# Kernel optimization log

Measured on AMD Instinct MI355X. Metric: run time of the kernel, lower is better.

## Reference

```python
import jax, jax.numpy as jnp
import numpy as np

N_NODES = 100000


def gcn_conv(x, W, b, row, col, n):
    """PyG GCNConv: linear transform, then symmetric-normalized aggregation
    with self-loops (add_self_loops=True, normalize=True, bias=True)."""
    h = x @ W  # [N, F_out]
    e_ones = jnp.ones(row.shape[0], dtype=x.dtype)
    # in-degree of target nodes, +1 for the implicit self-loop
    deg = jax.ops.segment_sum(e_ones, col, num_segments=n) + 1.0
    dinv = jax.lax.rsqrt(deg)  # deg >= 1 always
    norm = dinv[row] * dinv[col]  # [E]
    msg = h[row] * norm[:, None]  # gather + scale, [E, F_out]
    agg = jax.ops.segment_sum(msg, col, num_segments=n)  # scatter-add to targets
    agg = agg + h * (dinv * dinv)[:, None]  # self-loop contribution
    return agg + b


def setup_inputs() -> dict:
    key = jax.random.key(0)
    k1, k2, k3, k4 = jax.random.split(key, 4)
    F_in, F_hid, F_out = 512, 64, 40
    E = 1_600_000
    x = jax.random.normal(k1, (N_NODES, F_in), dtype=jnp.float32)
    edge_index = jax.random.randint(k2, (2, E), 0, N_NODES, dtype=jnp.int64)
    # Glorot-ish scaling for weights
    W1 = jax.random.normal(k3, (F_in, F_hid), dtype=jnp.float32) * (1.0 / np.sqrt(F_in))
    W2 = jax.random.normal(k4, (F_hid, F_out), dtype=jnp.float32) * (1.0 / np.sqrt(F_hid))
    b1 = jnp.zeros((F_hid,), dtype=jnp.float32)
    b2 = jnp.zeros((F_out,), dtype=jnp.float32)
    return {"x": x, "edge_index": edge_index, "W1": W1, "b1": b1, "W2": W2, "b2": b2}


def reference(x, edge_index, W1, b1, W2, b2):
    n = x.shape[0]
    row, col = edge_index[0], edge_index[1]
    h = jax.nn.relu(gcn_conv(x, W1, b1, row, col, n))
    # dropout is identity in eval mode (training=False)
    h = gcn_conv(h, W2, b2, row, col, n)
    return jax.nn.log_softmax(h, axis=1)
```

## Files before the change

kernel.cpp:

```cpp
#include <hip/hip_runtime.h>
#include <math.h>


#define FIN 512
#define FHID 64
#define FOUT 40

#define BSH 8
#define BN 256
#define BCAP 5120
#define EPW 4096

typedef __attribute__((ext_vector_type(8))) short short8;
typedef __attribute__((ext_vector_type(4))) float f32x4;
typedef unsigned short ushort_t;
typedef unsigned int uint_t;

__device__ __forceinline__ ushort_t bf16_rn(float f) {
    union { float f; uint_t u; } v; v.f = f;
    uint_t r = v.u + 0x7FFF + ((v.u >> 16) & 1);
    return (ushort_t)(r >> 16);
}
__device__ __forceinline__ uint_t pack_bf16(float a, float b) {
    return (uint_t)bf16_rn(a) | ((uint_t)bf16_rn(b) << 16);
}
__device__ __forceinline__ float bf16_to_f(ushort_t u) {
    union { uint_t i; float f; } t; t.i = ((uint_t)u) << 16; return t.f;
}
__device__ __forceinline__ void add8(float* acc, uint4 g) {
    acc[0] += __uint_as_float(g.x << 16);
    acc[1] += __uint_as_float(g.x & 0xFFFF0000u);
    acc[2] += __uint_as_float(g.y << 16);
    acc[3] += __uint_as_float(g.y & 0xFFFF0000u);
    acc[4] += __uint_as_float(g.z << 16);
    acc[5] += __uint_as_float(g.z & 0xFFFF0000u);
    acc[6] += __uint_as_float(g.w << 16);
    acc[7] += __uint_as_float(g.w & 0xFFFF0000u);
}

__global__ __launch_bounds__(256) void bucket_scatter_kernel(
    const int* __restrict__ row, const int* __restrict__ col,
    int* __restrict__ gcur, uint_t* __restrict__ stage, int E) {
    __shared__ uint_t cnt[512];
    __shared__ uint_t base[512];
    int tid = threadIdx.x;
    cnt[tid] = 0; cnt[tid + 256] = 0;
    __syncthreads();
    int e0 = blockIdx.x * EPW;
    int creg[16];
#pragma unroll
    for (int it = 0; it < 16; ++it) {
        int e = e0 + it * 256 + tid;
        creg[it] = (e < E) ? col[e] : -1;
        if (e < E) atomicAdd(&cnt[((uint_t)creg[it]) >> BSH], 1u);
    }
    __syncthreads();
    uint_t c0 = cnt[tid], c1 = cnt[tid + 256];
    base[tid] = c0 ? (uint_t)atomicAdd(&gcur[tid], (int)c0) : 0u;
    base[tid + 256] = c1 ? (uint_t)atomicAdd(&gcur[tid + 256], (int)c1) : 0u;
    __syncthreads();
    cnt[tid] = 0; cnt[tid + 256] = 0;
    __syncthreads();
#pragma unroll
    for (int it = 0; it < 16; ++it) {
        int e = e0 + it * 256 + tid;
        if (e < E) {
            int c = creg[it];
            int r = row[e];
            int b = c >> BSH;
            uint_t slot = base[b] + atomicAdd(&cnt[b], 1u);
            stage[(size_t)b * BCAP + slot] = ((uint_t)r << BSH) | (uint_t)(c & (BN - 1));
        }
    }
}

__global__ void scan2_kernel(int* __restrict__ bsums, int nb) {
    __shared__ int tmp[512];
    int tid = threadIdx.x;
    int v = (tid < nb) ? bsums[tid] : 0;
    tmp[tid] = v;
    __syncthreads();
    for (int off = 1; off < 512; off <<= 1) {
        int t = (tid >= off) ? tmp[tid - off] : 0;
        __syncthreads();
        tmp[tid] += t;
        __syncthreads();
    }
    if (tid < nb) bsums[tid] = tmp[tid] - v;
}

__global__ __launch_bounds__(256) void bucket_place_kernel(
    const int* __restrict__ gcur, const uint_t* __restrict__ stage,
    int* __restrict__ sSrc, int* __restrict__ deg, float* __restrict__ dinv,
    int* __restrict__ offs, int n) {
    __shared__ int lcnt[256];
    __shared__ int ltmp[256];
    __shared__ int lpos[256];
    int b = blockIdx.x, tid = threadIdx.x;
    int nodeBase = b << BSH;
    int bucketBase = gcur[b];
    int cnt = gcur[b + 1] - bucketBase;
    lcnt[tid] = 0;
    __syncthreads();
    const uint_t* sp = &stage[(size_t)b * BCAP];
    for (int i = tid; i < cnt; i += 256)
        atomicAdd(&lcnt[sp[i] & (BN - 1)], 1);
    __syncthreads();
    int v = lcnt[tid];
    ltmp[tid] = v;
    __syncthreads();
    for (int off = 1; off < 256; off <<= 1) {
        int t = (tid >= off) ? ltmp[tid - off] : 0;
        __syncthreads();
        ltmp[tid] += t;
        __syncthreads();
    }
    int gofs = bucketBase + ltmp[tid] - v;
    int node = nodeBase + tid;
    if (node < n) {
        deg[node] = v;
        dinv[node] = rsqrtf((float)v + 1.0f);
        offs[node] = gofs;
    }
    lpos[tid] = gofs;
    __syncthreads();
    for (int i = tid; i < cnt; i += 256) {
        uint_t w = sp[i];
        int pos = atomicAdd(&lpos[w & (BN - 1)], 1);
        sSrc[pos] = (int)(w >> BSH);
    }
}

__global__ void wprep_kernel(const float* __restrict__ W1, const float* __restrict__ W2,
                             ushort_t* __restrict__ Wt,
                             ushort_t* __restrict__ w2hi, ushort_t* __restrict__ w2lo) {
    int idx = blockIdx.x * 256 + threadIdx.x;
    if (idx < 32768) {
        int nrow = idx >> 9;
        int k = idx & 511;
        Wt[idx] = bf16_rn(W1[k * 64 + nrow]);
    } else if (idx < 32768 + 3072) {
        int i = idx - 32768;
        int j = i >> 6, k = i & 63;
        float w = (j < FOUT) ? W2[k * FOUT + j] : 0.f;
        ushort_t h = bf16_rn(w);
        w2hi[i] = h;
        w2lo[i] = bf16_rn(w - bf16_to_f(h));
    }
}

#define LDA 72
#define LDB 72
__global__ __launch_bounds__(256) void gemm1_kernel(
    const float* __restrict__ x, const ushort_t* __restrict__ Wt,
    const float* __restrict__ dinv, ushort_t* __restrict__ h1b, int n) {
    __shared__ ushort_t lA[128 * LDA];
    __shared__ ushort_t lB[64 * LDB];

    int tid = threadIdx.x;
    int wave = tid >> 6, lane = tid & 63;
    int quad = lane >> 4, m16 = lane & 15;
    int node0 = blockIdx.x * 128;

    int r0 = tid >> 4, k4 = tid & 15;
    int nr0 = tid >> 3, seg = tid & 7;

    f32x4 zero = {0.f, 0.f, 0.f, 0.f};
    f32x4 acc[2][4];
#pragma unroll
    for (int mt = 0; mt < 2; ++mt)
#pragma unroll
        for (int nt = 0; nt < 4; ++nt) acc[mt][nt] = zero;

    float4 ra[8];
    uint4 rb[2];

#pragma unroll
    for (int i = 0; i < 8; ++i) {
        int node = node0 + r0 + i * 16;
        float4 v = make_float4(0.f, 0.f, 0.f, 0.f);
        if (node < n) v = *reinterpret_cast<const float4*>(&x[(size_t)node * FIN + k4 * 4]);
        ra[i] = v;
    }
#pragma unroll
    for (int i = 0; i < 2; ++i)
        rb[i] = *reinterpret_cast<const uint4*>(&Wt[(size_t)(nr0 + i * 32) * FIN + seg * 8]);

    for (int c = 0; c < 8; ++c) {
#pragma unroll
        for (int i = 0; i < 8; ++i)
            *reinterpret_cast<uint2*>(&lA[(r0 + i * 16) * LDA + k4 * 4]) =
                make_uint2(pack_bf16(ra[i].x, ra[i].y), pack_bf16(ra[i].z, ra[i].w));
#pragma unroll
        for (int i = 0; i < 2; ++i)
            *reinterpret_cast<uint4*>(&lB[(nr0 + i * 32) * LDB + seg * 8]) = rb[i];
        __syncthreads();

        if (c < 7) {
            int kc = (c + 1) * 64;
#pragma unroll
            for (int i = 0; i < 8; ++i) {
                int node = node0 + r0 + i * 16;
                float4 v = make_float4(0.f, 0.f, 0.f, 0.f);
                if (node < n)
                    v = *reinterpret_cast<const float4*>(&x[(size_t)node * FIN + kc + k4 * 4]);
                ra[i] = v;
            }
#pragma unroll
            for (int i = 0; i < 2; ++i)
                rb[i] = *reinterpret_cast<const uint4*>(
                    &Wt[(size_t)(nr0 + i * 32) * FIN + kc + seg * 8]);
        }

#pragma unroll
        for (int kk = 0; kk < 2; ++kk) {
            short8 a[2], b[4];
#pragma unroll
            for (int mt = 0; mt < 2; ++mt)
                a[mt] = *reinterpret_cast<const short8*>(
                    &lA[(wave * 32 + mt * 16 + m16) * LDA + kk * 32 + quad * 8]);
#pragma unroll
            for (int nt = 0; nt < 4; ++nt)
                b[nt] = *reinterpret_cast<const short8*>(
                    &lB[(nt * 16 + m16) * LDB + kk * 32 + quad * 8]);
#pragma unroll
            for (int mt = 0; mt < 2; ++mt)
#pragma unroll
                for (int nt = 0; nt < 4; ++nt)
                    acc[mt][nt] = __builtin_amdgcn_mfma_f32_16x16x32_bf16(
                        a[mt], b[nt], acc[mt][nt], 0, 0, 0);
        }
        __syncthreads();
    }

#pragma unroll
    for (int mt = 0; mt < 2; ++mt) {
#pragma unroll
        for (int reg = 0; reg < 4; ++reg) {
            int node = node0 + wave * 32 + mt * 16 + quad * 4 + reg;
            if (node < n) {
                float di = dinv[node];
#pragma unroll
                for (int nt = 0; nt < 4; ++nt)
                    h1b[(size_t)node * 64 + nt * 16 + m16] =
                        bf16_rn(acc[mt][nt][reg] * di);
            }
        }
    }
}

template <int MODE>
__global__ __launch_bounds__(256) void agg_kernel(
    const int* __restrict__ offs, const int* __restrict__ deg,
    const int* __restrict__ sSrc, const ushort_t* __restrict__ src,
    const float* __restrict__ dinv, const float* __restrict__ b1,
    ushort_t* __restrict__ dst, int n) {
    __shared__ float lacc[8][4 * 68];
    __shared__ float lb1[64];
    int tid = threadIdx.x;
    if (MODE == 0 && tid < 64) lb1[tid] = b1[tid];

    int wv = tid >> 6, lane = tid & 63;
    int half = lane >> 5;
    int l32 = lane & 31;
    int e4 = l32 >> 3, c = l32 & 7;
    int slot = wv * 2 + half;
    int node = blockIdx.x * 8 + slot;
    bool valid = node < n;
    int start = valid ? offs[node] : 0;
    int cnt = valid ? deg[node] : 0;

    float acc[8];
#pragma unroll
    for (int j = 0; j < 8; ++j) acc[j] = 0.f;

    for (int base = 0; base < cnt; base += 16) {
        int i0 = base + e4, i1 = i0 + 4, i2 = i0 + 8, i3 = i0 + 12;
        int s0 = (i0 < cnt) ? sSrc[start + i0] : n;
        int s1 = (i1 < cnt) ? sSrc[start + i1] : n;
        int s2 = (i2 < cnt) ? sSrc[start + i2] : n;
        int s3 = (i3 < cnt) ? sSrc[start + i3] : n;
        uint4 g0 = *reinterpret_cast<const uint4*>(&src[(size_t)s0 * 64 + c * 8]);
        uint4 g1 = *reinterpret_cast<const uint4*>(&src[(size_t)s1 * 64 + c * 8]);
        uint4 g2 = *reinterpret_cast<const uint4*>(&src[(size_t)s2 * 64 + c * 8]);
        uint4 g3 = *reinterpret_cast<const uint4*>(&src[(size_t)s3 * 64 + c * 8]);
        add8(acc, g0);
        add8(acc, g1);
        add8(acc, g2);
        add8(acc, g3);
    }

    {
        float* lw = &lacc[slot][e4 * 68 + c * 8];
        *reinterpret_cast<float4*>(lw) = make_float4(acc[0], acc[1], acc[2], acc[3]);
        *reinterpret_cast<float4*>(lw + 4) = make_float4(acc[4], acc[5], acc[6], acc[7]);
    }
    __syncthreads();

    int s = tid >> 5;
    int fp = tid & 31;
    int enode = blockIdx.x * 8 + s;
    if (enode < n) {
        float sum0 = 0.f, sum1 = 0.f;
#pragma unroll
        for (int g = 0; g < 4; ++g) {
            sum0 += lacc[s][g * 68 + fp * 2];
            sum1 += lacc[s][g * 68 + fp * 2 + 1];
        }
        float di = dinv[enode];
        uint_t sv = *reinterpret_cast<const uint_t*>(&src[(size_t)enode * 64 + fp * 2]);
        float self0 = __uint_as_float(sv << 16);
        float self1 = __uint_as_float(sv & 0xFFFF0000u);
        float v0 = (sum0 + self0) * di;
        float v1 = (sum1 + self1) * di;
        if (MODE == 0) {
            v0 = fmaxf(v0 + lb1[fp * 2], 0.f) * di;
            v1 = fmaxf(v1 + lb1[fp * 2 + 1], 0.f) * di;
        }
        *reinterpret_cast<uint_t*>(&dst[(size_t)enode * 64 + fp * 2]) = pack_bf16(v0, v1);
    }
}

#define LDC 72
__global__ __launch_bounds__(256) void gemm2sm_kernel(
    const ushort_t* __restrict__ A, const ushort_t* __restrict__ w2hi,
    const ushort_t* __restrict__ w2lo, const float* __restrict__ b2,
    float* __restrict__ out, int n) {
    __shared__ ushort_t lA[128 * LDC];
    __shared__ ushort_t lBh[48 * LDC];
    __shared__ ushort_t lBl[48 * LDC];

    int tid = threadIdx.x;
    int wave = tid >> 6, lane = tid & 63;
    int quad = lane >> 4, m16 = lane & 15;
    int node0 = blockIdx.x * 128;

    {
        int r = tid & 127, part = tid >> 7;
        int node = node0 + r;
        uint4 z = make_uint4(0u, 0u, 0u, 0u);
        const uint4* sp = reinterpret_cast<const uint4*>(&A[(size_t)node * 64 + part * 32]);
#pragma unroll
        for (int i = 0; i < 4; ++i) {
            uint4 v = (node < n) ? sp[i] : z;
            *reinterpret_cast<uint4*>(&lA[r * LDC + part * 32 + i * 8]) = v;
        }
    }
    for (int i = tid; i < 384; i += 256) {
        int row = i >> 3, seg = i & 7;
        *reinterpret_cast<uint4*>(&lBh[row * LDC + seg * 8]) =
            reinterpret_cast<const uint4*>(w2hi)[i];
        *reinterpret_cast<uint4*>(&lBl[row * LDC + seg * 8]) =
            reinterpret_cast<const uint4*>(w2lo)[i];
    }
    float rb2_0 = b2[m16];
    float rb2_1 = b2[16 + m16];
    float rb2_2 = (m16 < 8) ? b2[32 + m16] : 0.f;
    __syncthreads();

    f32x4 zero = {0.f, 0.f, 0.f, 0.f};
    f32x4 acc[2][3];
#pragma unroll
    for (int mt = 0; mt < 2; ++mt)
#pragma unroll
        for (int nt = 0; nt < 3; ++nt) acc[mt][nt] = zero;

#pragma unroll
    for (int kk = 0; kk < 2; ++kk) {
        short8 a[2], bh[3], bl[3];
#pragma unroll
        for (int mt = 0; mt < 2; ++mt)
            a[mt] = *reinterpret_cast<const short8*>(
                &lA[(wave * 32 + mt * 16 + m16) * LDC + kk * 32 + quad * 8]);
#pragma unroll
        for (int nt = 0; nt < 3; ++nt) {
            bh[nt] = *reinterpret_cast<const short8*>(
                &lBh[(nt * 16 + m16) * LDC + kk * 32 + quad * 8]);
            bl[nt] = *reinterpret_cast<const short8*>(
                &lBl[(nt * 16 + m16) * LDC + kk * 32 + quad * 8]);
        }
#pragma unroll
        for (int mt = 0; mt < 2; ++mt)
#pragma unroll
            for (int nt = 0; nt < 3; ++nt) {
                acc[mt][nt] = __builtin_amdgcn_mfma_f32_16x16x32_bf16(
                    a[mt], bh[nt], acc[mt][nt], 0, 0, 0);
                acc[mt][nt] = __builtin_amdgcn_mfma_f32_16x16x32_bf16(
                    a[mt], bl[nt], acc[mt][nt], 0, 0, 0);
            }
    }

    bool c2 = (m16 < 8);
#pragma unroll
    for (int mt = 0; mt < 2; ++mt) {
#pragma unroll
        for (int reg = 0; reg < 4; ++reg) {
            int node = node0 + wave * 32 + mt * 16 + quad * 4 + reg;
            float r0 = acc[mt][0][reg] + rb2_0;
            float r1 = acc[mt][1][reg] + rb2_1;
            float r2 = acc[mt][2][reg] + rb2_2;
            float pm = fmaxf(fmaxf(r0, r1), c2 ? r2 : -INFINITY);
#pragma unroll
            for (int mask = 1; mask <= 8; mask <<= 1)
                pm = fmaxf(pm, __shfl_xor(pm, mask));
            float s = expf(r0 - pm) + expf(r1 - pm) + (c2 ? expf(r2 - pm) : 0.f);
#pragma unroll
            for (int mask = 1; mask <= 8; mask <<= 1)
                s += __shfl_xor(s, mask);
            float ls = logf(s) + pm;
            if (node < n) {
                float* op = &out[(size_t)node * FOUT];
                op[m16] = r0 - ls;
                op[16 + m16] = r1 - ls;
                if (c2) op[32 + m16] = r2 - ls;
            }
        }
    }
}

extern "C" void kernel_launch(void* const* d_in, const int* in_sizes, int n_in,
                              void* d_out, int out_size, void* d_ws, size_t ws_size,
                              hipStream_t stream) {
    const float* x  = (const float*)d_in[0];
    const int*   ei = (const int*)d_in[1];
    const float* W1 = (const float*)d_in[2];
    const float* b1 = (const float*)d_in[3];
    const float* W2 = (const float*)d_in[4];
    const float* b2 = (const float*)d_in[5];
    float* out = (float*)d_out;

    int n = in_sizes[0] / FIN;
    int E = in_sizes[1] / 2;
    const int* row = ei;
    const int* col = ei + E;

    int* wsi = (int*)d_ws;
    const size_t NR = 100352;
    int*      deg   = wsi;
    float*    dinv  = (float*)(wsi + NR);
    int*      offs  = wsi + 2 * NR;
    int*      gcur  = wsi + 3 * NR;
    ushort_t* Wt    = (ushort_t*)(wsi + 3 * NR + 512);
    ushort_t* w2hi  = Wt + 64 * 512;
    ushort_t* w2lo  = w2hi + 48 * 64;
    uint_t*   stage = (uint_t*)(w2lo + 48 * 64);
    int*      sSrc  = (int*)(stage + (size_t)512 * BCAP);
    ushort_t* h1b   = (ushort_t*)(sSrc + (size_t)E);
    ushort_t* h1a   = h1b + (size_t)(n + 1) * 64;
    ushort_t* Abuf  = h1b;

    int NBUCK = (n + BN - 1) >> BSH;
    int nwg1 = (E + EPW - 1) / EPW;

    hipMemsetAsync(gcur, 0, 512 * 4, stream);
    hipMemsetAsync(h1b + (size_t)n * 64, 0, 128, stream);
    hipMemsetAsync(h1a + (size_t)n * 64, 0, 128, stream);
    bucket_scatter_kernel<<<nwg1, 256, 0, stream>>>(row, col, gcur, stage, E);
    scan2_kernel<<<1, 512, 0, stream>>>(gcur, 512);
    bucket_place_kernel<<<NBUCK, 256, 0, stream>>>(gcur, stage, sSrc, deg, dinv, offs, n);

    wprep_kernel<<<140, 256, 0, stream>>>(W1, W2, Wt, w2hi, w2lo);

    gemm1_kernel<<<(n + 127) / 128, 256, 0, stream>>>(x, Wt, dinv, h1b, n);

    agg_kernel<0><<<(n + 7) / 8, 256, 0, stream>>>(offs, deg, sSrc, h1b, dinv, b1, h1a, n);

    agg_kernel<1><<<(n + 7) / 8, 256, 0, stream>>>(offs, deg, sSrc, h1a, dinv, b1, Abuf, n);

    gemm2sm_kernel<<<(n + 127) / 128, 256, 0, stream>>>(Abuf, w2hi, w2lo, b2, out, n);
}
```

Measured before the change: 445.9 us.

## Fold memsets and bucket scan into existing kernels; add nontemporal loads/stores

Replaces the three hipMemsetAsync calls by zeroing the bucket counters and sentinel rows inside the weight-prep kernel, which now runs first. The separate single-block scan kernel is removed, and every bucket_place block recomputes the 512-entry prefix sum itself. Streaming accesses (x, edge indices, stage, sSrc, gemm2 input and output) now use nontemporal load/store builtins to reduce cache pollution. This cuts launch count and small dispatch gaps, at the cost of redundant scan work in each place block.

```diff
diff --git a/kernel.cpp b/kernel.cpp
--- a/kernel.cpp
+++ b/kernel.cpp
@@ -13,8 +13,10 @@
 
 typedef __attribute__((ext_vector_type(8))) short short8;
 typedef __attribute__((ext_vector_type(4))) float f32x4;
+typedef __attribute__((ext_vector_type(4))) float float4v;
 typedef unsigned short ushort_t;
 typedef unsigned int uint_t;
+typedef __attribute__((ext_vector_type(4))) uint_t uint4v;
 
 __device__ __forceinline__ ushort_t bf16_rn(float f) {
     union { float f; uint_t u; } v; v.f = f;
@@ -38,103 +40,14 @@
     acc[7] += __uint_as_float(g.w & 0xFFFF0000u);
 }
 
-__global__ __launch_bounds__(256) void bucket_scatter_kernel(
-    const int* __restrict__ row, const int* __restrict__ col,
-    int* __restrict__ gcur, uint_t* __restrict__ stage, int E) {
-    __shared__ uint_t cnt[512];
-    __shared__ uint_t base[512];
-    int tid = threadIdx.x;
-    cnt[tid] = 0; cnt[tid + 256] = 0;
-    __syncthreads();
-    int e0 = blockIdx.x * EPW;
-    int creg[16];
-#pragma unroll
-    for (int it = 0; it < 16; ++it) {
-        int e = e0 + it * 256 + tid;
-        creg[it] = (e < E) ? col[e] : -1;
-        if (e < E) atomicAdd(&cnt[((uint_t)creg[it]) >> BSH], 1u);
-    }
-    __syncthreads();
-    uint_t c0 = cnt[tid], c1 = cnt[tid + 256];
-    base[tid] = c0 ? (uint_t)atomicAdd(&gcur[tid], (int)c0) : 0u;
-    base[tid + 256] = c1 ? (uint_t)atomicAdd(&gcur[tid + 256], (int)c1) : 0u;
-    __syncthreads();
-    cnt[tid] = 0; cnt[tid + 256] = 0;
-    __syncthreads();
-#pragma unroll
-    for (int it = 0; it < 16; ++it) {
-        int e = e0 + it * 256 + tid;
-        if (e < E) {
-            int c = creg[it];
-            int r = row[e];
-            int b = c >> BSH;
-            uint_t slot = base[b] + atomicAdd(&cnt[b], 1u);
-            stage[(size_t)b * BCAP + slot] = ((uint_t)r << BSH) | (uint_t)(c & (BN - 1));
-        }
-    }
-}
-
-__global__ void scan2_kernel(int* __restrict__ bsums, int nb) {
-    __shared__ int tmp[512];
-    int tid = threadIdx.x;
-    int v = (tid < nb) ? bsums[tid] : 0;
-    tmp[tid] = v;
-    __syncthreads();
-    for (int off = 1; off < 512; off <<= 1) {
-        int t = (tid >= off) ? tmp[tid - off] : 0;
-        __syncthreads();
-        tmp[tid] += t;
-        __syncthreads();
-    }
-    if (tid < nb) bsums[tid] = tmp[tid] - v;
-}
-
-__global__ __launch_bounds__(256) void bucket_place_kernel(
-    const int* __restrict__ gcur, const uint_t* __restrict__ stage,
-    int* __restrict__ sSrc, int* __restrict__ deg, float* __restrict__ dinv,
-    int* __restrict__ offs, int n) {
-    __shared__ int lcnt[256];
-    __shared__ int ltmp[256];
-    __shared__ int lpos[256];
-    int b = blockIdx.x, tid = threadIdx.x;
-    int nodeBase = b << BSH;
-    int bucketBase = gcur[b];
-    int cnt = gcur[b + 1] - bucketBase;
-    lcnt[tid] = 0;
-    __syncthreads();
-    const uint_t* sp = &stage[(size_t)b * BCAP];
-    for (int i = tid; i < cnt; i += 256)
-        atomicAdd(&lcnt[sp[i] & (BN - 1)], 1);
-    __syncthreads();
-    int v = lcnt[tid];
-    ltmp[tid] = v;
-    __syncthreads();
-    for (int off = 1; off < 256; off <<= 1) {
-        int t = (tid >= off) ? ltmp[tid - off] : 0;
-        __syncthreads();
-        ltmp[tid] += t;
-        __syncthreads();
-    }
-    int gofs = bucketBase + ltmp[tid] - v;
-    int node = nodeBase + tid;
-    if (node < n) {
-        deg[node] = v;
-        dinv[node] = rsqrtf((float)v + 1.0f);
-        offs[node] = gofs;
-    }
-    lpos[tid] = gofs;
-    __syncthreads();
-    for (int i = tid; i < cnt; i += 256) {
-        uint_t w = sp[i];
-        int pos = atomicAdd(&lpos[w & (BN - 1)], 1);
-        sSrc[pos] = (int)(w >> BSH);
-    }
-}
-
 __global__ void wprep_kernel(const float* __restrict__ W1, const float* __restrict__ W2,
                              ushort_t* __restrict__ Wt,
-                             ushort_t* __restrict__ w2hi, ushort_t* __restrict__ w2lo) {
+                             ushort_t* __restrict__ w2hi, ushort_t* __restrict__ w2lo,
+                             int* __restrict__ gcur,
+                             ushort_t* __restrict__ sent1, ushort_t* __restrict__ sent2) {
     int idx = blockIdx.x * 256 + threadIdx.x;
+    if (idx < 512) gcur[idx] = 0;
+    if (idx < 64) { sent1[idx] = 0; sent2[idx] = 0; }
     if (idx < 32768) {
         int nrow = idx >> 9;
         int k = idx & 511;
@@ -149,6 +62,96 @@
     }
 }
 
+__global__ __launch_bounds__(256) void bucket_scatter_kernel(
+    const int* __restrict__ row, const int* __restrict__ col,
+    int* __restrict__ gcur, uint_t* __restrict__ stage, int E) {
+    __shared__ uint_t cnt[512];
+    __shared__ uint_t base[512];
+    int tid = threadIdx.x;
+    cnt[tid] = 0; cnt[tid + 256] = 0;
+    __syncthreads();
+    int e0 = blockIdx.x * EPW;
+    int creg[16];
+#pragma unroll
+    for (int it = 0; it < 16; ++it) {
+        int e = e0 + it * 256 + tid;
+        creg[it] = (e < E) ? __builtin_nontemporal_load(&col[e]) : -1;
+        if (e < E) atomicAdd(&cnt[((uint_t)creg[it]) >> BSH], 1u);
+    }
+    __syncthreads();
+    uint_t c0 = cnt[tid], c1 = cnt[tid + 256];
+    base[tid] = c0 ? (uint_t)atomicAdd(&gcur[tid], (int)c0) : 0u;
+    base[tid + 256] = c1 ? (uint_t)atomicAdd(&gcur[tid + 256], (int)c1) : 0u;
+    __syncthreads();
+    cnt[tid] = 0; cnt[tid + 256] = 0;
+    __syncthreads();
+#pragma unroll
+    for (int it = 0; it < 16; ++it) {
+        int e = e0 + it * 256 + tid;
+        if (e < E) {
+            int c = creg[it];
+            int r = __builtin_nontemporal_load(&row[e]);
+            int b = c >> BSH;
+            uint_t slot = base[b] + atomicAdd(&cnt[b], 1u);
+            stage[(size_t)b * BCAP + slot] = ((uint_t)r << BSH) | (uint_t)(c & (BN - 1));
+        }
+    }
+}
+
+__global__ __launch_bounds__(256) void bucket_place_kernel(
+    const int* __restrict__ gcur, const uint_t* __restrict__ stage,
+    int* __restrict__ sSrc, int* __restrict__ deg, float* __restrict__ dinv,
+    int* __restrict__ offs, int n) {
+    __shared__ int sc[512];
+    __shared__ int lcnt[256];
+    __shared__ int ltmp[256];
+    __shared__ int lpos[256];
+    int b = blockIdx.x, tid = threadIdx.x;
+    int i1 = tid + 256;
+    sc[tid] = gcur[tid];
+    sc[i1] = gcur[i1];
+    __syncthreads();
+    for (int off = 1; off < 512; off <<= 1) {
+        int a0 = (tid >= off) ? sc[tid - off] : 0;
+        int a1 = (i1 >= off) ? sc[i1 - off] : 0;
+        __syncthreads();
+        sc[tid] += a0; sc[i1] += a1;
+        __syncthreads();
+    }
+    int cntB = gcur[b];
+    int bucketBase = sc[b] - cntB;
+    int nodeBase = b << BSH;
+    lcnt[tid] = 0;
+    __syncthreads();
+    const uint_t* sp = &stage[(size_t)b * BCAP];
+    for (int i = tid; i < cntB; i += 256)
+        atomicAdd(&lcnt[__builtin_nontemporal_load(&sp[i]) & (BN - 1)], 1);
+    __syncthreads();
+    int v = lcnt[tid];
+    ltmp[tid] = v;
+    __syncthreads();
+    for (int off = 1; off < 256; off <<= 1) {
+        int t = (tid >= off) ? ltmp[tid - off] : 0;
+        __syncthreads();
+        ltmp[tid] += t;
+        __syncthreads();
+    }
+    int gofs = bucketBase + ltmp[tid] - v;
+    int node = nodeBase + tid;
+    if (node < n) {
+        deg[node] = v;
+        dinv[node] = rsqrtf((float)v + 1.0f);
+        offs[node] = gofs;
+    }
+    lpos[tid] = gofs;
+    __syncthreads();
+    for (int i = tid; i < cntB; i += 256) {
+        uint_t w = __builtin_nontemporal_load(&sp[i]);
+        int pos = atomicAdd(&lpos[w & (BN - 1)], 1);
+        sSrc[pos] = (int)(w >> BSH);
+    }
+}
+
 #define LDA 72
 #define LDB 72
 __global__ __launch_bounds__(256) void gemm1_kernel(
@@ -172,14 +175,16 @@
 #pragma unroll
         for (int nt = 0; nt < 4; ++nt) acc[mt][nt] = zero;
 
-    float4 ra[8];
+    float4v ra[8];
     uint4 rb[2];
 
 #pragma unroll
     for (int i = 0; i < 8; ++i) {
         int node = node0 + r0 + i * 16;
-        float4 v = make_float4(0.f, 0.f, 0.f, 0.f);
-        if (node < n) v = *reinterpret_cast<const float4*>(&x[(size_t)node * FIN + k4 * 4]);
+        float4v v = {0.f, 0.f, 0.f, 0.f};
+        if (node < n)
+            v = __builtin_nontemporal_load(
+                reinterpret_cast<const float4v*>(&x[(size_t)node * FIN + k4 * 4]));
         ra[i] = v;
     }
 #pragma unroll
@@ -190,7 +195,7 @@
 #pragma unroll
         for (int i = 0; i < 8; ++i)
             *reinterpret_cast<uint2*>(&lA[(r0 + i * 16) * LDA + k4 * 4]) =
-                make_uint2(pack_bf16(ra[i].x, ra[i].y), pack_bf16(ra[i].z, ra[i].w));
+                make_uint2(pack_bf16(ra[i][0], ra[i][1]), pack_bf16(ra[i][2], ra[i][3]));
 #pragma unroll
         for (int i = 0; i < 2; ++i)
             *reinterpret_cast<uint4*>(&lB[(nr0 + i * 32) * LDB + seg * 8]) = rb[i];
@@ -201,9 +206,10 @@
 #pragma unroll
             for (int i = 0; i < 8; ++i) {
                 int node = node0 + r0 + i * 16;
-                float4 v = make_float4(0.f, 0.f, 0.f, 0.f);
+                float4v v = {0.f, 0.f, 0.f, 0.f};
                 if (node < n)
-                    v = *reinterpret_cast<const float4*>(&x[(size_t)node * FIN + kc + k4 * 4]);
+                    v = __builtin_nontemporal_load(
+                        reinterpret_cast<const float4v*>(&x[(size_t)node * FIN + kc + k4 * 4]));
                 ra[i] = v;
             }
 #pragma unroll
@@ -276,10 +282,10 @@
 
     for (int base = 0; base < cnt; base += 16) {
         int i0 = base + e4, i1 = i0 + 4, i2 = i0 + 8, i3 = i0 + 12;
-        int s0 = (i0 < cnt) ? sSrc[start + i0] : n;
-        int s1 = (i1 < cnt) ? sSrc[start + i1] : n;
-        int s2 = (i2 < cnt) ? sSrc[start + i2] : n;
-        int s3 = (i3 < cnt) ? sSrc[start + i3] : n;
+        int s0 = (i0 < cnt) ? __builtin_nontemporal_load(&sSrc[start + i0]) : n;
+        int s1 = (i1 < cnt) ? __builtin_nontemporal_load(&sSrc[start + i1]) : n;
+        int s2 = (i2 < cnt) ? __builtin_nontemporal_load(&sSrc[start + i2]) : n;
+        int s3 = (i3 < cnt) ? __builtin_nontemporal_load(&sSrc[start + i3]) : n;
         uint4 g0 = *reinterpret_cast<const uint4*>(&src[(size_t)s0 * 64 + c * 8]);
         uint4 g1 = *reinterpret_cast<const uint4*>(&src[(size_t)s1 * 64 + c * 8]);
         uint4 g2 = *reinterpret_cast<const uint4*>(&src[(size_t)s2 * 64 + c * 8]);
@@ -338,12 +344,12 @@
     {
         int r = tid & 127, part = tid >> 7;
         int node = node0 + r;
-        uint4 z = make_uint4(0u, 0u, 0u, 0u);
-        const uint4* sp = reinterpret_cast<const uint4*>(&A[(size_t)node * 64 + part * 32]);
+        uint4v z = {0u, 0u, 0u, 0u};
+        const uint4v* sp = reinterpret_cast<const uint4v*>(&A[(size_t)node * 64 + part * 32]);
 #pragma unroll
         for (int i = 0; i < 4; ++i) {
-            uint4 v = (node < n) ? sp[i] : z;
-            *reinterpret_cast<uint4*>(&lA[r * LDC + part * 32 + i * 8]) = v;
+            uint4v v = (node < n) ? __builtin_nontemporal_load(sp + i) : z;
+            *reinterpret_cast<uint4v*>(&lA[r * LDC + part * 32 + i * 8]) = v;
         }
     }
     for (int i = tid; i < 384; i += 256) {
@@ -410,9 +416,9 @@
             float ls = logf(s) + pm;
             if (node < n) {
                 float* op = &out[(size_t)node * FOUT];
-                op[m16] = r0 - ls;
-                op[16 + m16] = r1 - ls;
-                if (c2) op[32 + m16] = r2 - ls;
+                __builtin_nontemporal_store(r0 - ls, &op[m16]);
+                __builtin_nontemporal_store(r1 - ls, &op[16 + m16]);
+                if (c2) __builtin_nontemporal_store(r2 - ls, &op[32 + m16]);
             }
         }
     }
@@ -452,15 +458,12 @@
     int NBUCK = (n + BN - 1) >> BSH;
     int nwg1 = (E + EPW - 1) / EPW;
 
-    hipMemsetAsync(gcur, 0, 512 * 4, stream);
-    hipMemsetAsync(h1b + (size_t)n * 64, 0, 128, stream);
-    hipMemsetAsync(h1a + (size_t)n * 64, 0, 128, stream);
+    wprep_kernel<<<140, 256, 0, stream>>>(W1, W2, Wt, w2hi, w2lo, gcur,
+                                          h1b + (size_t)n * 64, h1a + (size_t)n * 64);
+
     bucket_scatter_kernel<<<nwg1, 256, 0, stream>>>(row, col, gcur, stage, E);
-    scan2_kernel<<<1, 512, 0, stream>>>(gcur, 512);
     bucket_place_kernel<<<NBUCK, 256, 0, stream>>>(gcur, stage, sSrc, deg, dinv, offs, n);
 
-    wprep_kernel<<<140, 256, 0, stream>>>(W1, W2, Wt, w2hi, w2lo);
-
     gemm1_kernel<<<(n + 127) / 128, 256, 0, stream>>>(x, Wt, dinv, h1b, n);
 
     agg_kernel<0><<<(n + 7) / 8, 256, 0, stream>>>(offs, deg, sSrc, h1b, dinv, b1, h1a, n);
```

Measured after the change: 432.1 us. 3.1% less time.
